# Kernel optimization log

Hardware: AMD Instinct MI355X
Metric: run time of the kernel (lower is better)

## Reference

```python
import jax, jax.numpy as jnp
import numpy as np

D = 1024
B, S_IMG, S_CTX = 2, 4096, 512
EPS = 1e-6


def rmsnorm(x, eps=1e-6):
    return x * jax.lax.rsqrt(jnp.mean(x * x, axis=-1, keepdims=True) + eps)


def layernorm(x, eps=1e-6):
    mu = jnp.mean(x, axis=-1, keepdims=True)
    var = jnp.mean((x - mu) ** 2, axis=-1, keepdims=True)
    return (x - mu) * jax.lax.rsqrt(var + eps)


def act_quant(x):
    # per-token 8-bit absmax quant
    scale = 127.0 / jnp.clip(jnp.max(jnp.abs(x), axis=-1, keepdims=True), 1e-5)
    return jnp.clip(jnp.round(x * scale), -128, 127) / scale


def weight_quant(w):
    # ternary (1.58-bit) absmean quant
    scale = 1.0 / jnp.clip(jnp.mean(jnp.abs(w)), 1e-5)
    return jnp.clip(jnp.round(w * scale), -1, 1) / scale


def bitlinear(x, w):
    # BitNet: RMSNorm -> STE activation quant, STE ternary weight quant
    xn = rmsnorm(x)
    xq = xn + jax.lax.stop_gradient(act_quant(xn) - xn)
    wq = w + jax.lax.stop_gradient(weight_quant(w) - w)
    return jnp.einsum('bsd,od->bso', xq, wq)


def ada_ln_zero(x, emb, w, b):
    e = (jax.nn.silu(emb) @ w.T + b)[:, None, :]  # [B,1,6D]
    scale_msa, shift_msa, gate_msa, scale_mlp, shift_mlp, gate_mlp = jnp.split(e, 6, axis=2)
    xn = layernorm(x) * (1.0 + scale_msa) + shift_msa
    return xn, gate_msa, shift_mlp, scale_mlp, gate_mlp


def hgrn_bit_attention(x, wi, wf, wg, wo, gnorm_w):
    i = bitlinear(x, wi)
    f = jax.nn.sigmoid(bitlinear(x, wf))
    i = jax.nn.silu(i) * (1.0 - f)  # swiglu(i, 1-f)
    # elementwise linear recurrence h_t = f_t * h_{t-1} + i_t over seq dim
    def step(h, xs):
        i_t, f_t = xs
        h = f_t * h + i_t
        return h, h
    _, o = jax.lax.scan(step, jnp.zeros_like(i[:, 0]), (i.transpose(1, 0, 2), f.transpose(1, 0, 2)))
    o = o.transpose(1, 0, 2)  # [B,S,D]
    g = bitlinear(x, wg)
    o = rmsnorm(o) * gnorm_w * (g * jax.nn.sigmoid(g))  # RMSNorm + swish gate
    return bitlinear(o, wo)


def bit_mlp(x, w_gate, w_down):
    y = bitlinear(x, w_gate)
    gate, y = jnp.split(y, 2, axis=-1)
    return bitlinear(jax.nn.silu(gate) * y, w_down)


def flux_block(hidden_states, encoder_hidden_states, temb,
               adaln_w, adaln_b, adaln_ctx_w, adaln_ctx_b,
               attn_wi, attn_wf, attn_wg, attn_wo, attn_gnorm_w,
               ff_wgate, ff_wdown, ffc_wgate, ffc_wdown):
    nh, gate_msa, shift_mlp, scale_mlp, gate_mlp = ada_ln_zero(hidden_states, temb, adaln_w, adaln_b)
    nc, c_gate_msa, c_shift_mlp, c_scale_mlp, c_gate_mlp = ada_ln_zero(encoder_hidden_states, temb, adaln_ctx_w, adaln_ctx_b)
    len_c = nc.shape[1]
    joint = jnp.concatenate([nc, nh], axis=1)
    attn_out = hgrn_bit_attention(joint, attn_wi, attn_wf, attn_wg, attn_wo, attn_gnorm_w)
    c_attn, x_attn = attn_out[:, :len_c], attn_out[:, len_c:]

    hidden_states = hidden_states + gate_msa * x_attn
    nh2 = layernorm(hidden_states) * (1.0 + scale_mlp) + shift_mlp
    hidden_states = hidden_states + gate_mlp * bit_mlp(nh2, ff_wgate, ff_wdown)

    encoder_hidden_states = encoder_hidden_states + c_gate_msa * c_attn
    nc2 = layernorm(encoder_hidden_states) * (1.0 + c_scale_mlp) + c_shift_mlp
    encoder_hidden_states = encoder_hidden_states + c_gate_mlp * bit_mlp(nc2, ffc_wgate, ffc_wdown)
    return hidden_states, encoder_hidden_states


def setup_inputs() -> dict:
    key = jax.random.key(0)
    ks = jax.random.split(key, 16)
    w = lambda k, shape: jax.random.normal(k, shape, jnp.float32) * 0.02
    return {
        'hidden_states': jax.random.normal(ks[0], (B, S_IMG, D), jnp.float32),
        'encoder_hidden_states': jax.random.normal(ks[1], (B, S_CTX, D), jnp.float32),
        'temb': jax.random.normal(ks[2], (B, D), jnp.float32),
        'adaln_w': w(ks[3], (6 * D, D)), 'adaln_b': jnp.zeros((6 * D,), jnp.float32),
        'adaln_ctx_w': w(ks[4], (6 * D, D)), 'adaln_ctx_b': jnp.zeros((6 * D,), jnp.float32),
        'attn_wi': w(ks[5], (D, D)), 'attn_wf': w(ks[6], (D, D)),
        'attn_wg': w(ks[7], (D, D)), 'attn_wo': w(ks[8], (D, D)),
        'attn_gnorm_w': jnp.ones((D,), jnp.float32),
        'ff_wgate': w(ks[9], (8 * D, D)), 'ff_wdown': w(ks[10], (D, 4 * D)),
        'ffc_wgate': w(ks[11], (8 * D, D)), 'ffc_wdown': w(ks[12], (D, 4 * D)),
    }


def reference(hidden_states, encoder_hidden_states, temb,
              adaln_w, adaln_b, adaln_ctx_w, adaln_ctx_b,
              attn_wi, attn_wf, attn_wg, attn_wo, attn_gnorm_w,
              ff_wgate, ff_wdown, ffc_wgate, ffc_wdown):
    return flux_block(hidden_states, encoder_hidden_states, temb,
                      adaln_w, adaln_b, adaln_ctx_w, adaln_ctx_b,
                      attn_wi, attn_wf, attn_wg, attn_wo, attn_gnorm_w,
                      ff_wgate, ff_wdown, ffc_wgate, ffc_wdown)
```

## Files before the change

### kernel.cpp

```cpp
#include <hip/hip_runtime.h>
#include <hip/hip_bf16.h>
#include <stdint.h>

#define DM   1024
#define SJ   4608
#define SCTX 512
#define SIMG 4096
#define NCH  512
#define TCH  9

typedef __attribute__((ext_vector_type(4))) int   i32x4;
typedef __attribute__((ext_vector_type(4))) float f32x4;

__device__ __forceinline__ float bf2f(unsigned short u){
  union { unsigned int i; float f; } v; v.i = ((unsigned int)u) << 16; return v.f;
}
__device__ __forceinline__ unsigned short f2bf(float f){
  unsigned int u = __float_as_uint(f);
  u += 0x7fffu + ((u >> 16) & 1u);
  return (unsigned short)(u >> 16);
}
__device__ __forceinline__ float sigm(float x){ return 1.f/(1.f+__expf(-x)); }
__device__ __forceinline__ signed char q8(float v, float lo, float hi){
  return (signed char)(int)fminf(fmaxf(rintf(v),lo),hi);
}

__device__ __forceinline__ float wsum(float v){
  #pragma unroll
  for(int o=32;o>0;o>>=1) v += __shfl_xor(v,o);
  return v;
}
__device__ __forceinline__ float wmax(float v){
  #pragma unroll
  for(int o=32;o>0;o>>=1) v = fmaxf(v,__shfl_xor(v,o));
  return v;
}
__device__ __forceinline__ void blockSumSum(float& a, float& b, float* s1, float* s2){
  a = wsum(a); b = wsum(b);
  if(!(threadIdx.x&63)){ s1[threadIdx.x>>6]=a; s2[threadIdx.x>>6]=b; }
  __syncthreads();
  a = s1[0]+s1[1]+s1[2]+s1[3];
  b = s2[0]+s2[1]+s2[2]+s2[3];
  __syncthreads();
}
__device__ __forceinline__ void blockSumMax(float& a, float& b, float* s1, float* s2){
  a = wsum(a); b = wmax(b);
  if(!(threadIdx.x&63)){ s1[threadIdx.x>>6]=a; s2[threadIdx.x>>6]=b; }
  __syncthreads();
  a = s1[0]+s1[1]+s1[2]+s1[3];
  b = fmaxf(fmaxf(s2[0],s2[1]),fmaxf(s2[2],s2[3]));
  __syncthreads();
}

typedef __attribute__((address_space(1))) void gvoid_t;
typedef __attribute__((address_space(3))) void lvoid_t;
__device__ __forceinline__ void gl_lds16(const void* g, void* l){
  __builtin_amdgcn_global_load_lds((gvoid_t*)g, (lvoid_t*)l, 16, 0, 0);
}

struct WList {
  const float* w[8];
  unsigned long long n[8];
  signed char* q[8];
};

__global__ __launch_bounds__(256)
void wq_reduce(WList L, float* __restrict__ part){
  __shared__ float s1[4];
  int m = blockIdx.y;
  const float4* w4 = (const float4*)L.w[m];
  size_t n4 = L.n[m] >> 2;
  float s = 0.f;
  for(size_t i = (size_t)blockIdx.x*256 + threadIdx.x; i < n4; i += (size_t)512*256){
    float4 v = w4[i];
    s += fabsf(v.x)+fabsf(v.y)+fabsf(v.z)+fabsf(v.w);
  }
  s = wsum(s);
  if(!(threadIdx.x&63)) s1[threadIdx.x>>6] = s;
  __syncthreads();
  if(!threadIdx.x) part[m*512 + blockIdx.x] = s1[0]+s1[1]+s1[2]+s1[3];
}

__global__ __launch_bounds__(256)
void wq_finalize(WList L, const float* __restrict__ part, float* __restrict__ swinv){
  __shared__ float s1[4];
  int m = blockIdx.x;
  float s = part[m*512 + threadIdx.x] + part[m*512 + 256 + threadIdx.x];
  s = wsum(s);
  if(!(threadIdx.x&63)) s1[threadIdx.x>>6] = s;
  __syncthreads();
  if(!threadIdx.x){
    float mean = (s1[0]+s1[1]+s1[2]+s1[3]) / (float)L.n[m];
    swinv[m] = fmaxf(mean, 1e-5f);
  }
}

__global__ __launch_bounds__(256)
void wq_quant(WList L, const float* __restrict__ swinv){
  int m = blockIdx.y;
  float sc = 1.f / swinv[m];
  const float4* w4 = (const float4*)L.w[m];
  signed char* q = L.q[m];
  size_t n4 = L.n[m] >> 2;
  for(size_t i = (size_t)blockIdx.x*256 + threadIdx.x; i < n4; i += (size_t)1024*256){
    float4 v = w4[i];
    char4 o;
    o.x = q8(v.x*sc,-1.f,1.f);
    o.y = q8(v.y*sc,-1.f,1.f);
    o.z = q8(v.z*sc,-1.f,1.f);
    o.w = q8(v.w*sc,-1.f,1.f);
    ((char4*)q)[i] = o;
  }
}

__global__ __launch_bounds__(256)
void adaln_gemv(const float* __restrict__ temb, const float* __restrict__ W,
                const float* __restrict__ bias, float* __restrict__ e){
  int o = blockIdx.x*4 + (threadIdx.x>>6);
  int b = blockIdx.y;
  int lane = threadIdx.x & 63;
  const float4* t4 = (const float4*)(temb + b*DM);
  const float4* w4 = (const float4*)(W + (size_t)o*DM);
  float acc = 0.f;
  #pragma unroll
  for(int i=0;i<4;i++){
    float4 tv = t4[i*64+lane], wv = w4[i*64+lane];
    acc += (tv.x*sigm(tv.x))*wv.x + (tv.y*sigm(tv.y))*wv.y
         + (tv.z*sigm(tv.z))*wv.z + (tv.w*sigm(tv.w))*wv.w;
  }
  acc = wsum(acc);
  if(!lane) e[b*6144 + o] = acc + bias[o];
}

__global__ __launch_bounds__(256)
void modnorm_quant(const float* __restrict__ x, int bshift,
                   const float* __restrict__ e, int scaleOff, int shiftOff,
                   signed char* __restrict__ xq, float* __restrict__ rsx,
                   int outRowOff, int outBatchStride){
  __shared__ float s1[4], s2[4];
  const int tid = threadIdx.x;
  const int row = blockIdx.x;
  const int b = row >> bshift, s = row & ((1<<bshift)-1);
  float4 xv = ((const float4*)(x + (size_t)row*DM))[tid];
  float sum = xv.x+xv.y+xv.z+xv.w;
  float ss  = xv.x*xv.x+xv.y*xv.y+xv.z*xv.z+xv.w*xv.w;
  blockSumSum(sum, ss, s1, s2);
  float mu  = sum * (1.f/DM);
  float inv = rsqrtf(ss*(1.f/DM) - mu*mu + 1e-6f);
  float4 scv = ((const float4*)(e + b*6144 + scaleOff))[tid];
  float4 shv = ((const float4*)(e + b*6144 + shiftOff))[tid];
  float n0 = (xv.x-mu)*inv*(1.f+scv.x)+shv.x;
  float n1 = (xv.y-mu)*inv*(1.f+scv.y)+shv.y;
  float n2 = (xv.z-mu)*inv*(1.f+scv.z)+shv.z;
  float n3 = (xv.w-mu)*inv*(1.f+scv.w)+shv.w;
  float ss2 = n0*n0+n1*n1+n2*n2+n3*n3;
  float mx  = fmaxf(fmaxf(fabsf(n0),fabsf(n1)),fmaxf(fabsf(n2),fabsf(n3)));
  blockSumMax(ss2, mx, s1, s2);
  float rms   = rsqrtf(ss2*(1.f/DM) + 1e-6f);
  float amaxn = fmaxf(mx*rms, 1e-5f);
  float k     = rms*127.f/amaxn;
  int orow = b*outBatchStride + outRowOff + s;
  char4 q;
  q.x = q8(n0*k,-128.f,127.f);
  q.y = q8(n1*k,-128.f,127.f);
  q.z = q8(n2*k,-128.f,127.f);
  q.w = q8(n3*k,-128.f,127.f);
  ((char4*)(xq + (size_t)orow*DM))[tid] = q;
  if(!tid) rsx[orow] = amaxn*(1.f/127.f);
}

__global__ __launch_bounds__(256)
void resid_modnorm(const float* __restrict__ x, const unsigned short* __restrict__ attn,
                   int attnRowOff, int bshift,
                   const float* __restrict__ e,
                   float* __restrict__ hout,
                   signed char* __restrict__ xq, float* __restrict__ rsx){
  __shared__ float s1[4], s2[4];
  const int tid = threadIdx.x;
  const int row = blockIdx.x;
  const int b = row >> bshift, s = row & ((1<<bshift)-1);
  const int arow = b*SJ + attnRowOff + s;
  float4 xv = ((const float4*)(x + (size_t)row*DM))[tid];
  ushort4 av = ((const ushort4*)(attn + (size_t)arow*DM))[tid];
  float4 gv = ((const float4*)(e + b*6144 + 2*1024))[tid];
  float h0 = xv.x + gv.x*bf2f(av.x);
  float h1 = xv.y + gv.y*bf2f(av.y);
  float h2 = xv.z + gv.z*bf2f(av.z);
  float h3 = xv.w + gv.w*bf2f(av.w);
  ((float4*)(hout + (size_t)row*DM))[tid] = make_float4(h0,h1,h2,h3);
  float sum = h0+h1+h2+h3;
  float ss  = h0*h0+h1*h1+h2*h2+h3*h3;
  blockSumSum(sum, ss, s1, s2);
  float mu  = sum * (1.f/DM);
  float inv = rsqrtf(ss*(1.f/DM) - mu*mu + 1e-6f);
  float4 scv = ((const float4*)(e + b*6144 + 3*1024))[tid];
  float4 shv = ((const float4*)(e + b*6144 + 4*1024))[tid];
  float n0 = (h0-mu)*inv*(1.f+scv.x)+shv.x;
  float n1 = (h1-mu)*inv*(1.f+scv.y)+shv.y;
  float n2 = (h2-mu)*inv*(1.f+scv.z)+shv.z;
  float n3 = (h3-mu)*inv*(1.f+scv.w)+shv.w;
  float ss2 = n0*n0+n1*n1+n2*n2+n3*n3;
  float mx  = fmaxf(fmaxf(fabsf(n0),fabsf(n1)),fmaxf(fabsf(n2),fabsf(n3)));
  blockSumMax(ss2, mx, s1, s2);
  float rms   = rsqrtf(ss2*(1.f/DM) + 1e-6f);
  float amaxn = fmaxf(mx*rms, 1e-5f);
  float k     = rms*127.f/amaxn;
  char4 q;
  q.x = q8(n0*k,-128.f,127.f);
  q.y = q8(n1*k,-128.f,127.f);
  q.z = q8(n2*k,-128.f,127.f);
  q.w = q8(n3*k,-128.f,127.f);
  ((char4*)(xq + (size_t)row*DM))[tid] = q;
  if(!tid) rsx[row] = amaxn*(1.f/127.f);
}

__global__ __launch_bounds__(256)
void resid_out(const float* __restrict__ hnew, const unsigned short* __restrict__ mlp,
               const float* __restrict__ e, int bshift, float* __restrict__ out){
  const int tid = threadIdx.x;
  const int row = blockIdx.x;
  const int b = row >> bshift;
  float4 hv = ((const float4*)(hnew + (size_t)row*DM))[tid];
  ushort4 mv = ((const ushort4*)(mlp + (size_t)row*DM))[tid];
  float4 gv = ((const float4*)(e + b*6144 + 5*1024))[tid];
  float4 o;
  o.x = hv.x + gv.x*bf2f(mv.x);
  o.y = hv.y + gv.y*bf2f(mv.y);
  o.z = hv.z + gv.z*bf2f(mv.z);
  o.w = hv.w + gv.w*bf2f(mv.w);
  ((float4*)(out + (size_t)row*DM))[tid] = o;
}

__global__ __launch_bounds__(256)
void rmsq4096(const unsigned short* __restrict__ z, signed char* __restrict__ zq,
              float* __restrict__ rsx){
  __shared__ float s1[4], s2[4];
  const int tid = threadIdx.x;
  const unsigned short* zr = z + (size_t)blockIdx.x*4096;
  signed char* qr = zq + (size_t)blockIdx.x*4096;
  float v[16];
  #pragma unroll
  for(int i=0;i<4;i++){
    ushort4 u = ((const ushort4*)zr)[tid + i*256];
    v[i*4+0]=bf2f(u.x); v[i*4+1]=bf2f(u.y); v[i*4+2]=bf2f(u.z); v[i*4+3]=bf2f(u.w);
  }
  float ss=0.f, mx=0.f;
  #pragma unroll
  for(int i=0;i<16;i++){ ss += v[i]*v[i]; mx = fmaxf(mx, fabsf(v[i])); }
  blockSumMax(ss, mx, s1, s2);
  float rms   = rsqrtf(ss*(1.f/4096.f) + 1e-6f);
  float amaxn = fmaxf(mx*rms, 1e-5f);
  float k     = rms*127.f/amaxn;
  #pragma unroll
  for(int i=0;i<4;i++){
    char4 q;
    q.x = q8(v[i*4+0]*k,-128.f,127.f);
    q.y = q8(v[i*4+1]*k,-128.f,127.f);
    q.z = q8(v[i*4+2]*k,-128.f,127.f);
    q.w = q8(v[i*4+3]*k,-128.f,127.f);
    ((char4*)qr)[tid + i*256] = q;
  }
  if(!tid) rsx[blockIdx.x] = amaxn*(1.f/127.f);
}

__global__ __launch_bounds__(256)
void scan_pass1(const unsigned short* __restrict__ ir, const unsigned short* __restrict__ fr,
                float* __restrict__ A, float* __restrict__ B){
  int c = blockIdx.x, b = blockIdx.y;
  int d0 = threadIdx.x*4;
  size_t base = ((size_t)b*SJ + (size_t)c*TCH)*DM + d0;
  float a0=1,a1=1,a2=1,a3=1, h0=0,h1=0,h2=0,h3=0;
  #pragma unroll
  for(int t=0;t<TCH;t++){
    ushort4 iv = *(const ushort4*)(ir + base + (size_t)t*DM);
    ushort4 fv = *(const ushort4*)(fr + base + (size_t)t*DM);
    float f0=sigm(bf2f(fv.x)), f1=sigm(bf2f(fv.y)), f2=sigm(bf2f(fv.z)), f3=sigm(bf2f(fv.w));
    float x0=bf2f(iv.x), x1=bf2f(iv.y), x2=bf2f(iv.z), x3=bf2f(iv.w);
    float p0=x0*sigm(x0)*(1.f-f0), p1=x1*sigm(x1)*(1.f-f1);
    float p2=x2*sigm(x2)*(1.f-f2), p3=x3*sigm(x3)*(1.f-f3);
    h0=f0*h0+p0; h1=f1*h1+p1; h2=f2*h2+p2; h3=f3*h3+p3;
    a0*=f0; a1*=f1; a2*=f2; a3*=f3;
  }
  size_t idx = (size_t)c*2048 + b*1024 + d0;
  *(float4*)(A + idx) = make_float4(a0,a1,a2,a3);
  *(float4*)(B + idx) = make_float4(h0,h1,h2,h3);
}

__global__ __launch_bounds__(256)
void scan_pass2(const float* __restrict__ A, const float* __restrict__ B, float* __restrict__ H){
  int chain = blockIdx.x*256 + threadIdx.x;
  float h = 0.f;
  for(int c0=0;c0<NCH;c0+=8){
    float a[8], bb[8];
    #pragma unroll
    for(int u=0;u<8;u++){
      a[u]  = A[(size_t)(c0+u)*2048 + chain];
      bb[u] = B[(size_t)(c0+u)*2048 + chain];
    }
    #pragma unroll
    for(int u=0;u<8;u++){
      H[(size_t)(c0+u)*2048 + chain] = h;
      h = a[u]*h + bb[u];
    }
  }
}

__global__ __launch_bounds__(256)
void scan3_gnorm(const unsigned short* __restrict__ ir, const unsigned short* __restrict__ fr,
                 const float* __restrict__ H, const unsigned short* __restrict__ g,
                 const float* __restrict__ gnw,
                 signed char* __restrict__ xq, float* __restrict__ rsx){
  __shared__ float s1[4], s2[4];
  int c = blockIdx.x, b = blockIdx.y;
  const int tid = threadIdx.x;
  int d0 = tid*4;
  size_t base = ((size_t)b*SJ + (size_t)c*TCH)*DM + d0;
  float4 hv = *(const float4*)(H + (size_t)c*2048 + b*1024 + d0);
  float h0=hv.x, h1=hv.y, h2=hv.z, h3=hv.w;
  float4 wv = ((const float4*)gnw)[tid];
  #pragma unroll
  for(int t=0;t<TCH;t++){
    ushort4 iv = *(const ushort4*)(ir + base + (size_t)t*DM);
    ushort4 fv = *(const ushort4*)(fr + base + (size_t)t*DM);
    float f0=sigm(bf2f(fv.x)), f1=sigm(bf2f(fv.y)), f2=sigm(bf2f(fv.z)), f3=sigm(bf2f(fv.w));
    float x0=bf2f(iv.x), x1=bf2f(iv.y), x2=bf2f(iv.z), x3=bf2f(iv.w);
    float p0=x0*sigm(x0)*(1.f-f0), p1=x1*sigm(x1)*(1.f-f1);
    float p2=x2*sigm(x2)*(1.f-f2), p3=x3*sigm(x3)*(1.f-f3);
    h0=f0*h0+p0; h1=f1*h1+p1; h2=f2*h2+p2; h3=f3*h3+p3;
    float ss = h0*h0+h1*h1+h2*h2+h3*h3, dummy = 0.f;
    blockSumSum(ss, dummy, s1, s2);
    float rms = rsqrtf(ss*(1.f/DM) + 1e-6f);
    ushort4 gv = *(const ushort4*)(g + base + (size_t)t*DM);
    float g0=bf2f(gv.x), g1=bf2f(gv.y), g2=bf2f(gv.z), g3=bf2f(gv.w);
    float n0 = h0*rms*wv.x*(g0*sigm(g0));
    float n1 = h1*rms*wv.y*(g1*sigm(g1));
    float n2 = h2*rms*wv.z*(g2*sigm(g2));
    float n3 = h3*rms*wv.w*(g3*sigm(g3));
    float ss2 = n0*n0+n1*n1+n2*n2+n3*n3;
    float mx  = fmaxf(fmaxf(fabsf(n0),fabsf(n1)),fmaxf(fabsf(n2),fabsf(n3)));
    blockSumMax(ss2, mx, s1, s2);
    float rms2  = rsqrtf(ss2*(1.f/DM) + 1e-6f);
    float amaxn = fmaxf(mx*rms2, 1e-5f);
    float k     = rms2*127.f/amaxn;
    char4 q;
    q.x = q8(n0*k,-128.f,127.f);
    q.y = q8(n1*k,-128.f,127.f);
    q.z = q8(n2*k,-128.f,127.f);
    q.w = q8(n3*k,-128.f,127.f);
    size_t row = (size_t)b*SJ + (size_t)c*TCH + t;
    *(char4*)(xq + row*DM + d0) = q;
    if(!tid) rsx[row] = amaxn*(1.f/127.f);
  }
}

#define EPI_IFG    0
#define EPI_OUT    1
#define EPI_GLU    2

struct GemmP {
  const float* rsx;
  const float* swinv;
  unsigned short* outb;
  float* outf;
  const float* egate;
  int bshift;
  const signed char* w2;
};

template<int N>
__device__ __forceinline__ void vm_wait(){
  if constexpr(N==0)       asm volatile("s_waitcnt vmcnt(0)"  ::: "memory");
  else if constexpr(N==4)  asm volatile("s_waitcnt vmcnt(4)"  ::: "memory");
  else if constexpr(N==6)  asm volatile("s_waitcnt vmcnt(6)"  ::: "memory");
  else if constexpr(N==8)  asm volatile("s_waitcnt vmcnt(8)"  ::: "memory");
  else                     asm volatile("s_waitcnt vmcnt(12)" ::: "memory");
}

template<int VAR, int EPI, int SWZ>
__global__ __launch_bounds__(256, (VAR==2)?3:2)
void gemm8(const signed char* __restrict__ Aq, const signed char* __restrict__ Bq,
           int Ncols, int K, int lda, GemmP p){
  constexpr int BN   = (VAR==0)? 256 : 128;
  constexpr int NF   = (VAR==0)? 4 : 2;
  constexpr int NBF  = (VAR==1)? 4 : NF;
  constexpr int BH   = (VAR==0)? 128 : 64;
  constexpr int TB   = (VAR==2)? 16384 : 24576;
  constexpr int NC   = (VAR==2)? 4 : 6;
  __shared__ char lds[3*TB];

  const int tid = threadIdx.x, wn = tid>>6, lane = tid&63;
  const int nwg = gridDim.x*gridDim.y;
  const int id  = blockIdx.y*gridDim.x + blockIdx.x;
  int nb, mb;
  if constexpr (SWZ==1){
    const int x = id&7, j = id>>3;
    nb = x*4 + (j&3);
    mb = j>>2;
  } else {
    const int wg = (id&7)*(nwg>>3) + (id>>3);
    nb = wg % gridDim.x; mb = wg / gridDim.x;
  }

  const int sl = tid>>3;
  const int sd = (tid&7) ^ (sl&7);
  const int sdk = (sd&3)*16;
  const int sdh = sd>>2;
  const signed char* agp  = Aq + (size_t)(mb*128 + sl + sdh*64)*lda + sdk;
  const signed char* bg1p = Bq + (size_t)(nb*BN  + sl + sdh*BH)*lda + sdk;
  const signed char* bg2p = nullptr;
  if constexpr (VAR==1) bg2p = p.w2 + (size_t)(nb*128 + sl + sdh*64)*lda + sdk;

  auto stage = [&](char* buf, int k0){
    gl_lds16(agp + k0,           buf + tid*16);
    gl_lds16(agp + 32*lda + k0,  buf + 4096 + tid*16);
    if constexpr (VAR==0){
      gl_lds16(bg1p + k0,           buf + 8192  + tid*16);
      gl_lds16(bg1p + 32*lda + k0,  buf + 12288 + tid*16);
      gl_lds16(bg1p + 64*lda + k0,  buf + 16384 + tid*16);
      gl_lds16(bg1p + 96*lda + k0,  buf + 20480 + tid*16);
    } else if constexpr (VAR==1){
      gl_lds16(bg1p + k0,           buf + 8192  + tid*16);
      gl_lds16(bg1p + 32*lda + k0,  buf + 12288 + tid*16);
      gl_lds16(bg2p + k0,           buf + 16384 + tid*16);
      gl_lds16(bg2p + 32*lda + k0,  buf + 20480 + tid*16);
    } else {
      gl_lds16(bg1p + k0,           buf + 8192  + tid*16);
      gl_lds16(bg1p + 32*lda + k0,  buf + 12288 + tid*16);
    }
  };

  const int lr = lane&15, kq = lane>>4;
  int aoff[8];
  #pragma unroll
  for(int mf=0;mf<8;mf++){
    int R = mf*16 + lr;
    aoff[mf] = (R&63)*128 + ((((R>>6)<<2)|kq) ^ (R&7))*16;
  }
  int boff[NBF];
  if constexpr (VAR==0){
    #pragma unroll
    for(int nf=0;nf<4;nf++){
      int RB = wn*64 + nf*16 + lr;
      boff[nf] = 8192 + (RB&127)*128 + ((((RB>>7)<<2)|kq) ^ (RB&7))*16;
    }
  } else {
    #pragma unroll
    for(int m=0;m<((VAR==1)?2:1);m++){
      #pragma unroll
      for(int nf=0;nf<2;nf++){
        int RB = wn*32 + nf*16 + lr;
        boff[m*2+nf] = 8192 + m*8192 + (RB&63)*128 + ((((RB>>6)<<2)|kq) ^ (RB&7))*16;
      }
    }
  }

  i32x4 acc[8][NF];
  i32x4 acc2[(VAR==1)?8:1][NF];
  #pragma unroll
  for(int i=0;i<8;i++)
    #pragma unroll
    for(int j=0;j<NF;j++){ acc[i][j]=(i32x4){0,0,0,0}; if constexpr(VAR==1) acc2[i][j]=(i32x4){0,0,0,0}; }

  auto tileBody = [&](const char* buf){
    i32x4 af[8], bf_[NBF];
    #pragma unroll
    for(int mf=0;mf<8;mf++) af[mf] = *(const i32x4*)(buf + aoff[mf]);
    #pragma unroll
    for(int q=0;q<NBF;q++)  bf_[q] = *(const i32x4*)(buf + boff[q]);
    #pragma unroll
    for(int mf=0;mf<8;mf++){
      #pragma unroll
      for(int nf=0;nf<NF;nf++){
        acc[mf][nf] = __builtin_amdgcn_mfma_i32_16x16x64_i8(af[mf], bf_[nf], acc[mf][nf], 0,0,0);
        if constexpr (VAR==1)
          acc2[mf][nf] = __builtin_amdgcn_mfma_i32_16x16x64_i8(af[mf], bf_[NF+nf], acc2[mf][nf], 0,0,0);
      }
    }
  };

  char* bufA = lds;
  char* bufB = lds + TB;
  char* bufC = lds + 2*TB;
  stage(bufA, 0);
  stage(bufB, 64);
  const int NT = K>>6;
  for(int t=0; t<NT-2; ++t){
    stage(bufC, (t+2)<<6);
    vm_wait<2*NC>();
    __builtin_amdgcn_s_barrier();
    __builtin_amdgcn_sched_barrier(0);
    tileBody(bufA);
    __builtin_amdgcn_sched_barrier(0);
    __builtin_amdgcn_s_barrier();
    char* tmp = bufA; bufA = bufB; bufB = bufC; bufC = tmp;
  }
  vm_wait<NC>();
  __builtin_amdgcn_s_barrier();
  __builtin_amdgcn_sched_barrier(0);
  tileBody(bufA);
  __builtin_amdgcn_sched_barrier(0);
  __builtin_amdgcn_s_barrier();
  vm_wait<0>();
  __builtin_amdgcn_s_barrier();
  __builtin_amdgcn_sched_barrier(0);
  tileBody(bufB);

  float sw;
  if constexpr (EPI==EPI_IFG) sw = p.swinv[(nb*BN)>>10];
  else                        sw = *p.swinv;
  const int r0 = mb*128;
  const int c0 = nb*BN + wn*((VAR==0)?64:32);
  #pragma unroll
  for(int mf=0;mf<8;mf++){
    #pragma unroll
    for(int j=0;j<4;j++){
      int r = r0 + mf*16 + kq*4 + j;
      float rs = p.rsx[r]*sw;
      #pragma unroll
      for(int nf=0;nf<NF;nf++){
        int c = c0 + nf*16 + lr;
        float val = (float)acc[mf][nf][j]*rs;
        if constexpr (EPI==EPI_IFG){
          int mat = c >> 10;
          p.outb[(size_t)mat*9437184 + (size_t)r*1024 + (c&1023)] = f2bf(val);
        } else if constexpr (EPI==EPI_GLU){
          float v2 = (float)acc2[mf][nf][j]*rs;
          p.outb[(size_t)r*Ncols + c] = f2bf(val*sigm(val)*v2);
        } else {
          p.outb[(size_t)r*Ncols + c] = f2bf(val);
        }
      }
    }
  }
}

__global__ __launch_bounds__(256, 2)
void gemm_ra8(const signed char* __restrict__ Aq, const signed char* __restrict__ Wq,
              int K, int lda, GemmP p){
  __shared__ signed char As[128*128];
  __shared__ signed char Bs[128*128];
  const int tid = threadIdx.x;
  const int wave = tid>>6, lane = tid&63;
  const int nwg = gridDim.x*gridDim.y;
  const int id  = blockIdx.y*gridDim.x + blockIdx.x;
  const int wg  = (id&7)*(nwg>>3) + (id>>3);
  const int nb  = wg % gridDim.x, mb = wg / gridDim.x;
  const int wr = wave>>1, wc = wave&1;
  const int koff = blockIdx.z*K;

  const int grow = wave*8 + (lane>>3);
  const int gcol = (lane&7)*16;
  const signed char* ag = Aq + (size_t)(mb*128 + grow)*lda + koff + gcol;
  const signed char* bg = Wq + (size_t)(nb*128 + grow)*lda + koff + gcol;
  char* asl = (char*)As + wave*1024;
  char* bsl = (char*)Bs + wave*1024;

  i32x4 acc[4][4];
  #pragma unroll
  for(int i=0;i<4;i++)
    #pragma unroll
    for(int j=0;j<4;j++) acc[i][j] = (i32x4){0,0,0,0};

  const int lrow = lane&15, kq = lane>>4;
  const signed char* arow = &As[(wr*64 + lrow)*128 + kq*16];
  const signed char* brow = &Bs[(wc*64 + lrow)*128 + kq*16];

  for(int k0=0; k0<K; k0+=128){
    #pragma unroll
    for(int pp=0;pp<4;pp++){
      gl_lds16(ag + (size_t)pp*32*lda + k0, asl + pp*4096);
      gl_lds16(bg + (size_t)pp*32*lda + k0, bsl + pp*4096);
    }
    __syncthreads();
    #pragma unroll
    for(int kk=0;kk<2;kk++){
      i32x4 af[4], bfr[4];
      #pragma unroll
      for(int m=0;m<4;m++) af[m]  = *(const i32x4*)(arow + m*2048 + kk*64);
      #pragma unroll
      for(int n=0;n<4;n++) bfr[n] = *(const i32x4*)(brow + n*2048 + kk*64);
      #pragma unroll
      for(int m=0;m<4;m++)
        #pragma unroll
        for(int n=0;n<4;n++)
          acc[m][n] = __builtin_amdgcn_mfma_i32_16x16x64_i8(af[m], bfr[n], acc[m][n], 0,0,0);
    }
    __syncthreads();
  }

  const float sw = *p.swinv;
  const int r0 = mb*128 + wr*64, c0 = nb*128 + wc*64;
  #pragma unroll
  for(int m=0;m<4;m++){
    #pragma unroll
    for(int j=0;j<4;j++){
      int r = r0 + m*16 + kq*4 + j;
      float rs = p.rsx[r]*sw;
      #pragma unroll
      for(int n=0;n<4;n++){
        int c = c0 + n*16 + lrow;
        float val = (float)acc[m][n][j]*rs;
        int b = r >> p.bshift;
        size_t idx = (size_t)r*DM + c;
        atomicAdd(&p.outf[idx], p.egate[b*6144 + 5*1024 + c]*val);
      }
    }
  }
}

extern "C" void kernel_launch(void* const* d_in, const int* in_sizes, int n_in,
                              void* d_out, int out_size, void* d_ws, size_t ws_size,
                              hipStream_t stream){
  (void)in_sizes; (void)n_in; (void)out_size; (void)ws_size;
  const float* hidden   = (const float*)d_in[0];
  const float* enc      = (const float*)d_in[1];
  const float* temb     = (const float*)d_in[2];
  const float* adaln_w  = (const float*)d_in[3];
  const float* adaln_b  = (const float*)d_in[4];
  const float* adaln_cw = (const float*)d_in[5];
  const float* adaln_cb = (const float*)d_in[6];
  const float* wi  = (const float*)d_in[7];
  const float* wf  = (const float*)d_in[8];
  const float* wg  = (const float*)d_in[9];
  const float* wo  = (const float*)d_in[10];
  const float* gnw = (const float*)d_in[11];
  const float* ffg = (const float*)d_in[12];
  const float* ffd = (const float*)d_in[13];
  const float* fcg = (const float*)d_in[14];
  const float* fcd = (const float*)d_in[15];

  const size_t MB = 1024ull*1024ull;
  char* ws = (char*)d_ws;
  signed char* W8_IFG = (signed char*)(ws + 0*MB);
  signed char* W8_WO  = (signed char*)(ws + 3*MB);
  signed char* W8_FFG = (signed char*)(ws + 4*MB);
  signed char* W8_FFD = (signed char*)(ws + 12*MB);
  signed char* W8_FCG = (signed char*)(ws + 16*MB);
  signed char* W8_FCD = (signed char*)(ws + 24*MB);
  float* PART  = (float*)(ws + 28*MB);
  float* SWINV = (float*)(ws + 28*MB + 32*1024);
  float* EH    = (float*)(ws + 28*MB + 64*1024);
  float* EC    = (float*)(ws + 28*MB + 112*1024);
  float* RSX1  = (float*)(ws + 28*MB + 160*1024);
  float* RSX2  = (float*)(ws + 28*MB + 200*1024);
  float* RSX3  = (float*)(ws + 28*MB + 240*1024);
  float* RSXZ  = (float*)(ws + 28*MB + 280*1024);
  float* RSX4  = (float*)(ws + 28*MB + 320*1024);
  float* RSXZC = (float*)(ws + 28*MB + 328*1024);
  float* SCANA = (float*)(ws + 29*MB);
  float* SCANB = (float*)(ws + 33*MB);
  float* SCANH = (float*)(ws + 37*MB);
  signed char* XQ8 = (signed char*)(ws + 41*MB);
  unsigned short* IRAW = (unsigned short*)(ws + 51*MB);
  unsigned short* FRAW = (unsigned short*)(ws + 69*MB);
  unsigned short* GRAW = (unsigned short*)(ws + 87*MB);
  unsigned short* ATTN = (unsigned short*)(ws + 51*MB);
  signed char* SG8 = (signed char*)(ws + 51*MB);
  unsigned short* MLPH = (unsigned short*)(ws + 83*MB);
  float* HNEW = (float*)(ws + 105*MB);
  unsigned short* SGB = (unsigned short*)(ws + 137*MB);
  float* OUT_H = (float*)d_out;
  float* OUT_C = (float*)d_out + 8388608;

  WList L;
  L.w[0]=wi;  L.n[0]=1048576ull; L.q[0]=W8_IFG;
  L.w[1]=wf;  L.n[1]=1048576ull; L.q[1]=W8_IFG + 1048576;
  L.w[2]=wg;  L.n[2]=1048576ull; L.q[2]=W8_IFG + 2097152;
  L.w[3]=wo;  L.n[3]=1048576ull; L.q[3]=W8_WO;
  L.w[4]=ffg; L.n[4]=8388608ull; L.q[4]=W8_FFG;
  L.w[5]=ffd; L.n[5]=4194304ull; L.q[5]=W8_FFD;
  L.w[6]=fcg; L.n[6]=8388608ull; L.q[6]=W8_FCG;
  L.w[7]=fcd; L.n[7]=4194304ull; L.q[7]=W8_FCD;
  wq_reduce  <<<dim3(512,8), 256, 0, stream>>>(L, PART);
  wq_finalize<<<8,          256, 0, stream>>>(L, PART, SWINV);
  wq_quant   <<<dim3(1024,8),256, 0, stream>>>(L, SWINV);

  adaln_gemv<<<dim3(1536,2), 256, 0, stream>>>(temb, adaln_w,  adaln_b,  EH);
  adaln_gemv<<<dim3(1536,2), 256, 0, stream>>>(temb, adaln_cw, adaln_cb, EC);

  modnorm_quant<<<1024, 256, 0, stream>>>(enc,    9,  EC, 0, 1024, XQ8, RSX1, 0,   SJ);
  modnorm_quant<<<8192, 256, 0, stream>>>(hidden, 12, EH, 0, 1024, XQ8, RSX1, 512, SJ);

  GemmP p{};
  p.rsx = RSX1; p.swinv = SWINV; p.outb = IRAW;
  gemm8<0,EPI_IFG,0><<<dim3(12,72), 256, 0, stream>>>(XQ8, W8_IFG, 3072, 1024, 1024, p);

  scan_pass1<<<dim3(NCH,2), 256, 0, stream>>>(IRAW, FRAW, SCANA, SCANB);
  scan_pass2<<<8,           256, 0, stream>>>(SCANA, SCANB, SCANH);
  scan3_gnorm<<<dim3(NCH,2), 256, 0, stream>>>(IRAW, FRAW, SCANH, GRAW, gnw, XQ8, RSX2);

  GemmP pw{};
  pw.rsx = RSX2; pw.swinv = SWINV+3; pw.outb = ATTN;
  gemm8<2,EPI_OUT,0><<<dim3(8,72), 256, 0, stream>>>(XQ8, W8_WO, 1024, 1024, 1024, pw);

  resid_modnorm<<<8192, 256, 0, stream>>>(hidden, ATTN, 512, 12, EH, HNEW, XQ8, RSX3);
  resid_modnorm<<<1024, 256, 0, stream>>>(enc,    ATTN, 0,   9,  EC, OUT_C,
                                          XQ8 + (size_t)8192*1024, RSX4);

  GemmP pg{};
  pg.rsx = RSX3; pg.swinv = SWINV+4; pg.outb = SGB; pg.w2 = W8_FFG + (size_t)4096*1024;
  gemm8<1,EPI_GLU,1><<<dim3(32,64), 256, 0, stream>>>(XQ8, W8_FFG, 4096, 1024, 1024, pg);
  rmsq4096<<<8192, 256, 0, stream>>>(SGB, SG8, RSXZ);
  GemmP pd{};
  pd.rsx = RSXZ; pd.swinv = SWINV+5; pd.outb = MLPH;
  gemm8<2,EPI_OUT,0><<<dim3(8,64), 256, 0, stream>>>(SG8, W8_FFD, 1024, 4096, 4096, pd);
  resid_out<<<8192, 256, 0, stream>>>(HNEW, MLPH, EH, 12, OUT_H);

  GemmP pc{};
  pc.rsx = RSX4; pc.swinv = SWINV+6; pc.outb = SGB; pc.w2 = W8_FCG + (size_t)4096*1024;
  gemm8<1,EPI_GLU,1><<<dim3(32,8), 256, 0, stream>>>(XQ8 + (size_t)8192*1024, W8_FCG, 4096, 1024, 1024, pc);
  rmsq4096<<<1024, 256, 0, stream>>>(SGB, SG8, RSXZC);
  GemmP pe{};
  pe.rsx = RSXZC; pe.swinv = SWINV+7; pe.outf = OUT_C; pe.egate = EC; pe.bshift = 9;
  gemm_ra8<<<dim3(8,8,4), 256, 0, stream>>>(SG8, W8_FCD, 1024, 4096, pe);
}
```

Baseline: 470.8 us.

## Merge paired launches and fuse MLP residual into down-proj GEMM epilogue

Merges the two adaLN GEMV launches into one grid over both weight sets, and merges the separate encoder and image modnorm and resid_modnorm launches into single joint kernels. Adds an EPI_RESID epilogue to the down-projection GEMM so the gated residual add writes fp32 output directly. This drops the bf16 MLP intermediate and the separate resid_out pass. The aim is to cut launch count and an 8192-row read/write pass, at the cost of scattered fp32 residual loads and stores in the GEMM epilogue.

Result: no change. 468.2 us (-0.5%).

```diff
diff --git a/kernel.cpp b/kernel.cpp
--- a/kernel.cpp
+++ b/kernel.cpp
@@ -114,8 +114,12 @@
 }
 
 __global__ __launch_bounds__(256)
-void adaln_gemv(const float* __restrict__ temb, const float* __restrict__ W,
-                const float* __restrict__ bias, float* __restrict__ e){
+void adaln_gemv2(const float* __restrict__ temb,
+                 const float* __restrict__ W1, const float* __restrict__ B1, float* __restrict__ E1,
+                 const float* __restrict__ W2, const float* __restrict__ B2, float* __restrict__ E2){
+  const float* W  = blockIdx.z ? W2 : W1;
+  const float* bs = blockIdx.z ? B2 : B1;
+  float* e        = blockIdx.z ? E2 : E1;
   int o = blockIdx.x*4 + (threadIdx.x>>6);
   int b = blockIdx.y;
   int lane = threadIdx.x & 63;
@@ -129,26 +133,33 @@
          + (tv.z*sigm(tv.z))*wv.z + (tv.w*sigm(tv.w))*wv.w;
   }
   acc = wsum(acc);
-  if(!lane) e[b*6144 + o] = acc + bias[o];
-}
-
-__global__ __launch_bounds__(256)
-void modnorm_quant(const float* __restrict__ x, int bshift,
-                   const float* __restrict__ e, int scaleOff, int shiftOff,
-                   signed char* __restrict__ xq, float* __restrict__ rsx,
-                   int outRowOff, int outBatchStride){
+  if(!lane) e[b*6144 + o] = acc + bs[o];
+}
+
+__global__ __launch_bounds__(256)
+void modnorm_joint(const float* __restrict__ enc, const float* __restrict__ hidden,
+                   const float* __restrict__ EC, const float* __restrict__ EH,
+                   signed char* __restrict__ xq, float* __restrict__ rsx){
   __shared__ float s1[4], s2[4];
   const int tid = threadIdx.x;
   const int row = blockIdx.x;
-  const int b = row >> bshift, s = row & ((1<<bshift)-1);
-  float4 xv = ((const float4*)(x + (size_t)row*DM))[tid];
+  const float* x; const float* e; int orow;
+  if (row < 1024){
+    int b = row >> 9, s = row & 511;
+    x = enc + (size_t)row*DM; e = EC + b*6144; orow = b*SJ + s;
+  } else {
+    int r2 = row - 1024;
+    int b = r2 >> 12, s = r2 & 4095;
+    x = hidden + (size_t)r2*DM; e = EH + b*6144; orow = b*SJ + 512 + s;
+  }
+  float4 xv = ((const float4*)x)[tid];
   float sum = xv.x+xv.y+xv.z+xv.w;
   float ss  = xv.x*xv.x+xv.y*xv.y+xv.z*xv.z+xv.w*xv.w;
   blockSumSum(sum, ss, s1, s2);
   float mu  = sum * (1.f/DM);
   float inv = rsqrtf(ss*(1.f/DM) - mu*mu + 1e-6f);
-  float4 scv = ((const float4*)(e + b*6144 + scaleOff))[tid];
-  float4 shv = ((const float4*)(e + b*6144 + shiftOff))[tid];
+  float4 scv = ((const float4*)(e + 0))[tid];
+  float4 shv = ((const float4*)(e + 1024))[tid];
   float n0 = (xv.x-mu)*inv*(1.f+scv.x)+shv.x;
   float n1 = (xv.y-mu)*inv*(1.f+scv.y)+shv.y;
   float n2 = (xv.z-mu)*inv*(1.f+scv.z)+shv.z;
@@ -159,7 +170,6 @@
   float rms   = rsqrtf(ss2*(1.f/DM) + 1e-6f);
   float amaxn = fmaxf(mx*rms, 1e-5f);
   float k     = rms*127.f/amaxn;
-  int orow = b*outBatchStride + outRowOff + s;
   char4 q;
   q.x = q8(n0*k,-128.f,127.f);
   q.y = q8(n1*k,-128.f,127.f);
@@ -170,31 +180,42 @@
 }
 
 __global__ __launch_bounds__(256)
-void resid_modnorm(const float* __restrict__ x, const unsigned short* __restrict__ attn,
-                   int attnRowOff, int bshift,
-                   const float* __restrict__ e,
-                   float* __restrict__ hout,
-                   signed char* __restrict__ xq, float* __restrict__ rsx){
+void resid_modnorm_joint(const float* __restrict__ hidden, const float* __restrict__ enc,
+                         const unsigned short* __restrict__ attn,
+                         const float* __restrict__ EH, const float* __restrict__ EC,
+                         float* __restrict__ HNEW, float* __restrict__ OUTC,
+                         signed char* __restrict__ xqi, signed char* __restrict__ xqc,
+                         float* __restrict__ rsxi, float* __restrict__ rsxc){
   __shared__ float s1[4], s2[4];
   const int tid = threadIdx.x;
   const int row = blockIdx.x;
-  const int b = row >> bshift, s = row & ((1<<bshift)-1);
-  const int arow = b*SJ + attnRowOff + s;
-  float4 xv = ((const float4*)(x + (size_t)row*DM))[tid];
+  const float* x; const float* e; float* hout; signed char* xq; float* rsx;
+  int arow, lrow;
+  if (row < 1024){
+    int b = row >> 9, s = row & 511;
+    x = enc + (size_t)row*DM; e = EC + b*6144; hout = OUTC + (size_t)row*DM;
+    xq = xqc; rsx = rsxc; lrow = row; arow = b*SJ + s;
+  } else {
+    int r2 = row - 1024;
+    int b = r2 >> 12, s = r2 & 4095;
+    x = hidden + (size_t)r2*DM; e = EH + b*6144; hout = HNEW + (size_t)r2*DM;
+    xq = xqi; rsx = rsxi; lrow = r2; arow = b*SJ + 512 + s;
+  }
+  float4 xv = ((const float4*)x)[tid];
   ushort4 av = ((const ushort4*)(attn + (size_t)arow*DM))[tid];
-  float4 gv = ((const float4*)(e + b*6144 + 2*1024))[tid];
+  float4 gv = ((const float4*)(e + 2*1024))[tid];
   float h0 = xv.x + gv.x*bf2f(av.x);
   float h1 = xv.y + gv.y*bf2f(av.y);
   float h2 = xv.z + gv.z*bf2f(av.z);
   float h3 = xv.w + gv.w*bf2f(av.w);
-  ((float4*)(hout + (size_t)row*DM))[tid] = make_float4(h0,h1,h2,h3);
+  ((float4*)hout)[tid] = make_float4(h0,h1,h2,h3);
   float sum = h0+h1+h2+h3;
   float ss  = h0*h0+h1*h1+h2*h2+h3*h3;
   blockSumSum(sum, ss, s1, s2);
   float mu  = sum * (1.f/DM);
   float inv = rsqrtf(ss*(1.f/DM) - mu*mu + 1e-6f);
-  float4 scv = ((const float4*)(e + b*6144 + 3*1024))[tid];
-  float4 shv = ((const float4*)(e + b*6144 + 4*1024))[tid];
+  float4 scv = ((const float4*)(e + 3*1024))[tid];
+  float4 shv = ((const float4*)(e + 4*1024))[tid];
   float n0 = (h0-mu)*inv*(1.f+scv.x)+shv.x;
   float n1 = (h1-mu)*inv*(1.f+scv.y)+shv.y;
   float n2 = (h2-mu)*inv*(1.f+scv.z)+shv.z;
@@ -210,25 +231,8 @@
   q.y = q8(n1*k,-128.f,127.f);
   q.z = q8(n2*k,-128.f,127.f);
   q.w = q8(n3*k,-128.f,127.f);
-  ((char4*)(xq + (size_t)row*DM))[tid] = q;
-  if(!tid) rsx[row] = amaxn*(1.f/127.f);
-}
-
-__global__ __launch_bounds__(256)
-void resid_out(const float* __restrict__ hnew, const unsigned short* __restrict__ mlp,
-               const float* __restrict__ e, int bshift, float* __restrict__ out){
-  const int tid = threadIdx.x;
-  const int row = blockIdx.x;
-  const int b = row >> bshift;
-  float4 hv = ((const float4*)(hnew + (size_t)row*DM))[tid];
-  ushort4 mv = ((const ushort4*)(mlp + (size_t)row*DM))[tid];
-  float4 gv = ((const float4*)(e + b*6144 + 5*1024))[tid];
-  float4 o;
-  o.x = hv.x + gv.x*bf2f(mv.x);
-  o.y = hv.y + gv.y*bf2f(mv.y);
-  o.z = hv.z + gv.z*bf2f(mv.z);
-  o.w = hv.w + gv.w*bf2f(mv.w);
-  ((float4*)(out + (size_t)row*DM))[tid] = o;
+  ((char4*)(xq + (size_t)lrow*DM))[tid] = q;
+  if(!tid) rsx[lrow] = amaxn*(1.f/127.f);
 }
 
 __global__ __launch_bounds__(256)
@@ -356,12 +360,14 @@
 #define EPI_IFG    0
 #define EPI_OUT    1
 #define EPI_GLU    2
+#define EPI_RESID  3
 
 struct GemmP {
   const float* rsx;
   const float* swinv;
   unsigned short* outb;
   float* outf;
+  const float* resid;
   const float* egate;
   int bshift;
   const signed char* w2;
@@ -526,6 +532,10 @@
         } else if constexpr (EPI==EPI_GLU){
           float v2 = (float)acc2[mf][nf][j]*rs;
           p.outb[(size_t)r*Ncols + c] = f2bf(val*sigm(val)*v2);
+        } else if constexpr (EPI==EPI_RESID){
+          int b = r >> p.bshift;
+          size_t idx = (size_t)r*DM + c;
+          p.outf[idx] = p.resid[idx] + p.egate[b*6144 + 5*1024 + c]*val;
         } else {
           p.outb[(size_t)r*Ncols + c] = f2bf(val);
         }
@@ -656,7 +666,6 @@
   unsigned short* GRAW = (unsigned short*)(ws + 87*MB);
   unsigned short* ATTN = (unsigned short*)(ws + 51*MB);
   signed char* SG8 = (signed char*)(ws + 51*MB);
-  unsigned short* MLPH = (unsigned short*)(ws + 83*MB);
   float* HNEW = (float*)(ws + 105*MB);
   unsigned short* SGB = (unsigned short*)(ws + 137*MB);
   float* OUT_H = (float*)d_out;
@@ -675,11 +684,10 @@
   wq_finalize<<<8,          256, 0, stream>>>(L, PART, SWINV);
   wq_quant   <<<dim3(1024,8),256, 0, stream>>>(L, SWINV);
 
-  adaln_gemv<<<dim3(1536,2), 256, 0, stream>>>(temb, adaln_w,  adaln_b,  EH);
-  adaln_gemv<<<dim3(1536,2), 256, 0, stream>>>(temb, adaln_cw, adaln_cb, EC);
-
-  modnorm_quant<<<1024, 256, 0, stream>>>(enc,    9,  EC, 0, 1024, XQ8, RSX1, 0,   SJ);
-  modnorm_quant<<<8192, 256, 0, stream>>>(hidden, 12, EH, 0, 1024, XQ8, RSX1, 512, SJ);
+  adaln_gemv2<<<dim3(1536,2,2), 256, 0, stream>>>(temb, adaln_w, adaln_b, EH,
+                                                  adaln_cw, adaln_cb, EC);
+
+  modnorm_joint<<<9216, 256, 0, stream>>>(enc, hidden, EC, EH, XQ8, RSX1);
 
   GemmP p{};
   p.rsx = RSX1; p.swinv = SWINV; p.outb = IRAW;
@@ -693,18 +701,18 @@
   pw.rsx = RSX2; pw.swinv = SWINV+3; pw.outb = ATTN;
   gemm8<2,EPI_OUT,0><<<dim3(8,72), 256, 0, stream>>>(XQ8, W8_WO, 1024, 1024, 1024, pw);
 
-  resid_modnorm<<<8192, 256, 0, stream>>>(hidden, ATTN, 512, 12, EH, HNEW, XQ8, RSX3);
-  resid_modnorm<<<1024, 256, 0, stream>>>(enc,    ATTN, 0,   9,  EC, OUT_C,
-                                          XQ8 + (size_t)8192*1024, RSX4);
+  resid_modnorm_joint<<<9216, 256, 0, stream>>>(hidden, enc, ATTN, EH, EC,
+                                                HNEW, OUT_C,
+                                                XQ8, XQ8 + (size_t)8192*1024,
+                                                RSX3, RSX4);
 
   GemmP pg{};
   pg.rsx = RSX3; pg.swinv = SWINV+4; pg.outb = SGB; pg.w2 = W8_FFG + (size_t)4096*1024;
   gemm8<1,EPI_GLU,1><<<dim3(32,64), 256, 0, stream>>>(XQ8, W8_FFG, 4096, 1024, 1024, pg);
   rmsq4096<<<8192, 256, 0, stream>>>(SGB, SG8, RSXZ);
   GemmP pd{};
-  pd.rsx = RSXZ; pd.swinv = SWINV+5; pd.outb = MLPH;
-  gemm8<2,EPI_OUT,0><<<dim3(8,64), 256, 0, stream>>>(SG8, W8_FFD, 1024, 4096, 4096, pd);
-  resid_out<<<8192, 256, 0, stream>>>(HNEW, MLPH, EH, 12, OUT_H);
+  pd.rsx = RSXZ; pd.swinv = SWINV+5; pd.outf = OUT_H; pd.resid = HNEW; pd.egate = EH; pd.bshift = 12;
+  gemm8<2,EPI_RESID,0><<<dim3(8,64), 256, 0, stream>>>(SG8, W8_FFD, 1024, 4096, 4096, pd);
 
   GemmP pc{};
   pc.rsx = RSX4; pc.swinv = SWINV+6; pc.outb = SGB; pc.w2 = W8_FCG + (size_t)4096*1024;
```
